# Kernel tuning notes

Hardware: AMD Instinct MI355X
Metric: run time of the kernel (lower is better)

The kernel has to match this reference:

```python
import jax, jax.numpy as jnp
import numpy as np

N = 100000
E = 1600000
F_IN = 512
HID = 8
HEADS = 8
NUM_CLASSES = 40
NEG_SLOPE = 0.2


def setup_inputs() -> dict:
    key = jax.random.key(0)
    ks = jax.random.split(key, 12)
    x = jax.random.normal(ks[0], (N, F_IN), dtype=jnp.float32)
    edge_index = jax.random.randint(ks[1], (2, E), 0, N, dtype=jnp.int64)
    s1 = 1.0 / np.sqrt(F_IN)
    s2 = 1.0 / np.sqrt(HID * HEADS)
    W1 = jax.random.normal(ks[2], (F_IN, HEADS * HID), dtype=jnp.float32) * s1
    a_src1 = jax.random.normal(ks[3], (HEADS, HID), dtype=jnp.float32) * s1
    a_dst1 = jax.random.normal(ks[4], (HEADS, HID), dtype=jnp.float32) * s1
    b1 = jnp.zeros((HEADS * HID,), dtype=jnp.float32)
    W2 = jax.random.normal(ks[5], (HEADS * HID, NUM_CLASSES), dtype=jnp.float32) * s2
    a_src2 = jax.random.normal(ks[6], (1, NUM_CLASSES), dtype=jnp.float32) * s2
    a_dst2 = jax.random.normal(ks[7], (1, NUM_CLASSES), dtype=jnp.float32) * s2
    b2 = jnp.zeros((NUM_CLASSES,), dtype=jnp.float32)
    return {"x": x, "edge_index": edge_index, "W1": W1, "a_src1": a_src1,
            "a_dst1": a_dst1, "b1": b1, "W2": W2, "a_src2": a_src2,
            "a_dst2": a_dst2, "b2": b2}


def _gat_conv(x, src, dst, W, a_src, a_dst, b, heads, out_ch):
    # linear projection, per-head: [N, heads, out_ch]
    h = (x @ W).reshape(N, heads, out_ch)
    # per-node attention logits [N, heads]
    al_s = jnp.einsum('nhf,hf->nh', h, a_src)
    al_d = jnp.einsum('nhf,hf->nh', h, a_dst)
    # per-edge raw scores [E', heads]
    e = jax.nn.leaky_relu(al_s[src] + al_d[dst], NEG_SLOPE)
    # segment softmax over edges sharing a destination node
    m = jax.lax.stop_gradient(jax.ops.segment_max(e, dst, num_segments=N))
    m = jnp.where(jnp.isfinite(m), m, 0.0)
    e = jnp.exp(e - m[dst])
    denom = jax.ops.segment_sum(e, dst, num_segments=N)
    alpha = e / denom[dst]  # [E', heads]
    # scatter-weighted aggregation of gathered source features
    out = jax.ops.segment_sum(alpha[:, :, None] * h[src], dst, num_segments=N)
    return out.reshape(N, heads * out_ch) + b


def reference(x, edge_index, W1, a_src1, a_dst1, b1, W2, a_src2, a_dst2, b2):
    # PyG GATConv default: add self-loops
    loops = jnp.arange(N, dtype=edge_index.dtype)
    src = jnp.concatenate([edge_index[0], loops])
    dst = jnp.concatenate([edge_index[1], loops])
    h = _gat_conv(x, src, dst, W1, a_src1, a_dst1, b1, HEADS, HID)
    h = jax.nn.elu(h)
    # dropout(p=0.6) is identity in eval mode
    out = _gat_conv(h, src, dst, W2, a_src2, a_dst2, b2, 1, NUM_CLASSES)
    return jax.nn.log_softmax(out, axis=1)
```

## Files before the change

kernel.cpp:

```cpp
#include <hip/hip_runtime.h>
#include <hip/hip_bf16.h>
#include <cstdint>
#include <cstddef>

#define N_NODES 100000
#define N_EDGES 1600000
#define E_TOT   (N_EDGES + N_NODES)
#define F_IN    512
#define HEADS   8
#define HID     8
#define F_H     64
#define NC      40
#define NEG     0.2f

#define BSH    8
#define NB     391
#define CHUNK  8192
#define NBLK_E ((E_TOT + CHUNK - 1) / CHUNK)
#define CAP    7168

typedef __attribute__((ext_vector_type(8))) __bf16 bf16x8;
typedef __attribute__((ext_vector_type(4))) float f32x4;
typedef __attribute__((ext_vector_type(8))) unsigned short u16x8;

__device__ __forceinline__ float bf2f(unsigned short u) {
  unsigned int w = ((unsigned int)u) << 16;
  return __builtin_bit_cast(float, w);
}
__device__ __forceinline__ unsigned short f2bf(float f) {
  __hip_bfloat16 b = __float2bfloat16(f);
  return __builtin_bit_cast(unsigned short, b);
}
__device__ __forceinline__ float lrexp(float v) {
  v = (v > 0.f) ? v : NEG * v;
  return __expf(v);
}

__global__ void k_detect(const int* __restrict__ ei, int* __restrict__ flag) {
  if (threadIdx.x == 0 && blockIdx.x == 0) {
    int nz = 0;
    for (int i = 0; i < 256; ++i) nz |= ei[2 * i + 1];
    *flag = (nz == 0) ? 1 : 0;
  }
}

__device__ __forceinline__ int load_dst(const int* __restrict__ ei, bool f, int i) {
  if (i < N_EDGES) return f ? ei[2 * (N_EDGES + i)] : ei[N_EDGES + i];
  return i - N_EDGES;
}
__device__ __forceinline__ int load_src(const int* __restrict__ ei, bool f, int i) {
  if (i < N_EDGES) return f ? ei[2 * i] : ei[i];
  return i - N_EDGES;
}

__global__ __launch_bounds__(256) void k_bhist(const int* __restrict__ ei,
                                               const int* __restrict__ flag,
                                               int* __restrict__ bcnt) {
  __shared__ int h[NB];
  const int t = threadIdx.x;
  for (int i = t; i < NB; i += 256) h[i] = 0;
  __syncthreads();
  const bool f = (*flag) != 0;
  const int base = blockIdx.x * CHUNK;
#pragma unroll
  for (int j = 0; j < CHUNK / 256; ++j) {
    int i = base + t + j * 256;
    if (i < E_TOT) atomicAdd(&h[load_dst(ei, f, i) >> BSH], 1);
  }
  __syncthreads();
  for (int i = t; i < NB; i += 256)
    if (h[i]) atomicAdd(&bcnt[i], h[i]);
}

__global__ __launch_bounds__(512) void k_bscan(const int* __restrict__ bcnt,
                                               int* __restrict__ bstart,
                                               int* __restrict__ bcur,
                                               int* __restrict__ rowstart) {
  __shared__ int sh[512];
  const int t = threadIdx.x;
  int v = (t < NB) ? bcnt[t] : 0;
  sh[t] = v;
  __syncthreads();
  for (int d = 1; d < 512; d <<= 1) {
    int u = (t >= d) ? sh[t - d] : 0;
    __syncthreads();
    sh[t] += u;
    __syncthreads();
  }
  if (t < NB) {
    int e = sh[t] - v;
    bstart[t] = e;
    bcur[t] = e;
  }
  if (t == 0) { bstart[NB] = E_TOT; rowstart[N_NODES] = E_TOT; }
}

__global__ __launch_bounds__(256) void k_bfill(const int* __restrict__ ei,
                                               const int* __restrict__ flag,
                                               int* __restrict__ bcur,
                                               unsigned int* __restrict__ inter) {
  __shared__ unsigned int ent[CHUNK];
  __shared__ int h[NB], ofs[NB], cur[NB], gpos[NB];
  const int t = threadIdx.x;
  const int base = blockIdx.x * CHUNK;
  const bool f = (*flag) != 0;
  for (int i = t; i < NB; i += 256) h[i] = 0;
  __syncthreads();
#pragma unroll
  for (int j = 0; j < CHUNK / 256; ++j) {
    int i = base + t + j * 256;
    if (i < E_TOT) atomicAdd(&h[load_dst(ei, f, i) >> BSH], 1);
  }
  __syncthreads();
  if (t < 64) {
    int loc[7];
    int s = 0;
#pragma unroll
    for (int k = 0; k < 7; ++k) {
      int idx = t * 7 + k;
      int hv = (idx < NB) ? h[idx] : 0;
      loc[k] = s;
      s += hv;
    }
    int incl = s;
    for (int dd = 1; dd < 64; dd <<= 1) {
      int u = __shfl_up(incl, dd);
      if (t >= dd) incl += u;
    }
    int excl = incl - s;
#pragma unroll
    for (int k = 0; k < 7; ++k) {
      int idx = t * 7 + k;
      if (idx < NB) ofs[idx] = excl + loc[k];
    }
  }
  __syncthreads();
  for (int i = t; i < NB; i += 256) {
    cur[i] = ofs[i];
    gpos[i] = h[i] ? atomicAdd(&bcur[i], h[i]) : 0;
  }
  __syncthreads();
#pragma unroll
  for (int j = 0; j < CHUNK / 256; ++j) {
    int i = base + t + j * 256;
    if (i < E_TOT) {
      int s = load_src(ei, f, i);
      int d = load_dst(ei, f, i);
      int p = atomicAdd(&cur[d >> BSH], 1);
      ent[p] = ((unsigned int)(d & 255) << 24) | (unsigned int)s;
    }
  }
  __syncthreads();
  const int wv = t >> 6, ln = t & 63;
  for (int b = wv; b < NB; b += 4) {
    int c = h[b];
    if (!c) continue;
    int g = gpos[b], o = ofs[b];
    for (int i = ln; i < c; i += 64) inter[g + i] = ent[o + i];
  }
}

__global__ __launch_bounds__(256) void k_cfill(const unsigned int* __restrict__ inter,
                                               const int* __restrict__ bstart,
                                               int* __restrict__ rowstart,
                                               int* __restrict__ csrc) {
  __shared__ unsigned int out_l[CAP];
  __shared__ int cnt[256], sc[256], cur2[256];
  const int t = threadIdx.x;
  const int b = blockIdx.x;
  const int segStart = bstart[b];
  const int L = bstart[b + 1] - segStart;
  cnt[t] = 0;
  __syncthreads();
  for (int i = t; i < L; i += 256) atomicAdd(&cnt[inter[segStart + i] >> 24], 1);
  __syncthreads();
  sc[t] = cnt[t];
  __syncthreads();
  for (int d = 1; d < 256; d <<= 1) {
    int v = (t >= d) ? sc[t - d] : 0;
    __syncthreads();
    sc[t] += v;
    __syncthreads();
  }
  const int excl = sc[t] - cnt[t];
  cur2[t] = excl;
  const int node = (b << BSH) + t;
  if (node < N_NODES) rowstart[node] = segStart + excl;
  __syncthreads();
  if (L <= CAP) {
    for (int i = t; i < L; i += 256) {
      unsigned int e = inter[segStart + i];
      int p = atomicAdd(&cur2[e >> 24], 1);
      out_l[p] = e & 0xFFFFFFu;
    }
    __syncthreads();
    for (int i = t; i < L; i += 256) csrc[segStart + i] = (int)out_l[i];
  } else {
    for (int i = t; i < L; i += 256) {
      unsigned int e = inter[segStart + i];
      int p = atomicAdd(&cur2[e >> 24], 1);
      csrc[segStart + p] = (int)(e & 0xFFFFFFu);
    }
  }
}

__global__ __launch_bounds__(256) void k_packW(const float* __restrict__ W1,
                                               uint4* __restrict__ w1f) {
  int tid = blockIdx.x * 256 + threadIdx.x;
  if (tid >= 4096) return;
  int lane = tid & 63;
  int t = (tid >> 6) & 3;
  int s = tid >> 8;
  int k0 = s * 32 + ((lane >> 4) << 3);
  int col = t * 16 + (lane & 15);
  u16x8 v;
#pragma unroll
  for (int i = 0; i < 8; ++i) v[i] = f2bf(W1[(size_t)(k0 + i) * F_H + col]);
  w1f[tid] = __builtin_bit_cast(uint4, v);
}

__global__ __launch_bounds__(256) void k_gemm1m(
    const float* __restrict__ x, const uint4* __restrict__ w1f,
    const float* __restrict__ a_src, const float* __restrict__ a_dst,
    unsigned short* __restrict__ h1b, float* __restrict__ als,
    float* __restrict__ ald) {
  const int t = threadIdx.x;
  const int lane = t & 63;
  const int wv = t >> 6;
  const int rb = blockIdx.x * 64 + wv * 16;
  int arow = rb + (lane & 15);
  if (arow >= N_NODES) arow = N_NODES - 1;
  const float* aptr = x + (size_t)arow * F_IN + ((lane >> 4) << 3);

  f32x4 acc[4];
#pragma unroll
  for (int i = 0; i < 4; ++i) acc[i] = (f32x4){0.f, 0.f, 0.f, 0.f};

#pragma unroll 4
  for (int s = 0; s < 16; ++s) {
    float4 a0 = *reinterpret_cast<const float4*>(aptr + s * 32);
    float4 a1 = *reinterpret_cast<const float4*>(aptr + s * 32 + 4);
    uint4 b0 = w1f[(s * 4 + 0) * 64 + lane];
    uint4 b1 = w1f[(s * 4 + 1) * 64 + lane];
    uint4 b2 = w1f[(s * 4 + 2) * 64 + lane];
    uint4 b3 = w1f[(s * 4 + 3) * 64 + lane];
    bf16x8 af;
    af[0] = (__bf16)a0.x; af[1] = (__bf16)a0.y;
    af[2] = (__bf16)a0.z; af[3] = (__bf16)a0.w;
    af[4] = (__bf16)a1.x; af[5] = (__bf16)a1.y;
    af[6] = (__bf16)a1.z; af[7] = (__bf16)a1.w;
    acc[0] = __builtin_amdgcn_mfma_f32_16x16x32_bf16(af, __builtin_bit_cast(bf16x8, b0), acc[0], 0, 0, 0);
    acc[1] = __builtin_amdgcn_mfma_f32_16x16x32_bf16(af, __builtin_bit_cast(bf16x8, b1), acc[1], 0, 0, 0);
    acc[2] = __builtin_amdgcn_mfma_f32_16x16x32_bf16(af, __builtin_bit_cast(bf16x8, b2), acc[2], 0, 0, 0);
    acc[3] = __builtin_amdgcn_mfma_f32_16x16x32_bf16(af, __builtin_bit_cast(bf16x8, b3), acc[3], 0, 0, 0);
  }

  const int r0 = rb + ((lane >> 4) << 2);
  const int c = lane & 15;
#pragma unroll
  for (int tt = 0; tt < 4; ++tt) {
#pragma unroll
    for (int i = 0; i < 4; ++i) {
      int r = r0 + i;
      if (r < N_NODES) h1b[(size_t)r * F_H + tt * 16 + c] = f2bf(acc[tt][i]);
    }
  }

  float asw[4], adw[4];
#pragma unroll
  for (int tt = 0; tt < 4; ++tt) {
    asw[tt] = a_src[tt * 16 + c];
    adw[tt] = a_dst[tt * 16 + c];
  }
  float sp[4][4], dp[4][4];
#pragma unroll
  for (int tt = 0; tt < 4; ++tt)
#pragma unroll
    for (int i = 0; i < 4; ++i) {
      sp[tt][i] = acc[tt][i] * asw[tt];
      dp[tt][i] = acc[tt][i] * adw[tt];
    }
#pragma unroll
  for (int dd = 1; dd < 8; dd <<= 1)
#pragma unroll
    for (int tt = 0; tt < 4; ++tt)
#pragma unroll
      for (int i = 0; i < 4; ++i) {
        sp[tt][i] += __shfl_xor(sp[tt][i], dd);
        dp[tt][i] += __shfl_xor(dp[tt][i], dd);
      }
  if ((c & 7) == 0) {
    const int hb = c >> 3;
#pragma unroll
    for (int i = 0; i < 4; ++i) {
      int r = r0 + i;
      if (r < N_NODES) {
#pragma unroll
        for (int tt = 0; tt < 4; ++tt) {
          als[(size_t)r * HEADS + tt * 2 + hb] = sp[tt][i];
          ald[(size_t)r * HEADS + tt * 2 + hb] = dp[tt][i];
        }
      }
    }
  }
}

__global__ __launch_bounds__(256) void k_agg1n(
    const int* __restrict__ rowstart, const int* __restrict__ csrc,
    const unsigned short* __restrict__ h1b, const float* __restrict__ als,
    const float* __restrict__ ald, const float* __restrict__ b1,
    unsigned short* __restrict__ hactb) {
  const int w = (int)((blockIdx.x * 256 + threadIdx.x) >> 6);
  const int lane = threadIdx.x & 63;
  const int grp = lane >> 3;
  const int l = lane & 7;
  const int n = w * 8 + grp;
  const bool live = (n < N_NODES);
  const int e0 = live ? rowstart[n] : 0;
  const int e1 = live ? rowstart[n + 1] : 0;
  const float aldv = live ? ald[(size_t)n * HEADS + l] : 0.f;

  float den = 0.f;
  float acc[8];
#pragma unroll
  for (int k = 0; k < 8; ++k) acc[k] = 0.f;

  int e = e0;
  for (; e + 4 <= e1; e += 4) {
    int4 sv = *reinterpret_cast<const int4*>(&csrc[e]);
    float a0 = als[(size_t)sv.x * HEADS + l];
    float a1 = als[(size_t)sv.y * HEADS + l];
    float a2 = als[(size_t)sv.z * HEADS + l];
    float a3 = als[(size_t)sv.w * HEADS + l];
    uint4 u0 = *reinterpret_cast<const uint4*>(&h1b[(size_t)sv.x * F_H + l * 8]);
    uint4 u1 = *reinterpret_cast<const uint4*>(&h1b[(size_t)sv.y * F_H + l * 8]);
    uint4 u2 = *reinterpret_cast<const uint4*>(&h1b[(size_t)sv.z * F_H + l * 8]);
    uint4 u3 = *reinterpret_cast<const uint4*>(&h1b[(size_t)sv.w * F_H + l * 8]);
    float p0 = lrexp(a0 + aldv), p1 = lrexp(a1 + aldv);
    float p2 = lrexp(a2 + aldv), p3 = lrexp(a3 + aldv);
    den += (p0 + p1) + (p2 + p3);
    const unsigned int* q0 = &u0.x;
    const unsigned int* q1 = &u1.x;
    const unsigned int* q2 = &u2.x;
    const unsigned int* q3 = &u3.x;
#pragma unroll
    for (int k = 0; k < 4; ++k) {
      acc[2 * k]     += p0 * bf2f((unsigned short)q0[k]) + p1 * bf2f((unsigned short)q1[k])
                      + p2 * bf2f((unsigned short)q2[k]) + p3 * bf2f((unsigned short)q3[k]);
      acc[2 * k + 1] += p0 * bf2f((unsigned short)(q0[k] >> 16)) + p1 * bf2f((unsigned short)(q1[k] >> 16))
                      + p2 * bf2f((unsigned short)(q2[k] >> 16)) + p3 * bf2f((unsigned short)(q3[k] >> 16));
    }
  }
  for (; e < e1; ++e) {
    int s = csrc[e];
    float a = als[(size_t)s * HEADS + l];
    uint4 u = *reinterpret_cast<const uint4*>(&h1b[(size_t)s * F_H + l * 8]);
    float p = lrexp(a + aldv);
    den += p;
    const unsigned int* q = &u.x;
#pragma unroll
    for (int k = 0; k < 4; ++k) {
      acc[2 * k]     += p * bf2f((unsigned short)q[k]);
      acc[2 * k + 1] += p * bf2f((unsigned short)(q[k] >> 16));
    }
  }

  if (live) {
    float inv = 1.f / den;
    uint4 outw;
    unsigned int* ow = &outw.x;
#pragma unroll
    for (int k = 0; k < 4; ++k) {
      float ox = acc[2 * k] * inv + b1[l * 8 + 2 * k];
      float oy = acc[2 * k + 1] * inv + b1[l * 8 + 2 * k + 1];
      ox = (ox > 0.f) ? ox : expm1f(ox);
      oy = (oy > 0.f) ? oy : expm1f(oy);
      ow[k] = ((unsigned int)f2bf(oy) << 16) | (unsigned int)f2bf(ox);
    }
    *reinterpret_cast<uint4*>(&hactb[(size_t)n * F_H + l * 8]) = outw;
  }
}

__global__ __launch_bounds__(256) void k_l2proj(
    const unsigned short* __restrict__ hactb, const float* __restrict__ W2,
    const float* __restrict__ a_src2, const float* __restrict__ a_dst2,
    unsigned short* __restrict__ h2b, float* __restrict__ als2,
    float* __restrict__ ald2) {
  __shared__ float hs[64 * 68];
  __shared__ float w2s[F_H * NC];
  const int t = threadIdx.x;
  const int nb = blockIdx.x * 64;
  {
    int r0 = t >> 3, c8 = t & 7;
#pragma unroll
    for (int i = 0; i < 2; ++i) {
      int r = r0 + i * 32;
      int gr = nb + r;
      u16x8 v = (u16x8)(0);
      if (gr < N_NODES)
        v = *reinterpret_cast<const u16x8*>(&hactb[(size_t)gr * F_H + c8 * 8]);
#pragma unroll
      for (int k = 0; k < 8; ++k) hs[r * 68 + c8 * 8 + k] = bf2f(v[k]);
    }
  }
  for (int i = t; i < F_H * NC; i += 256) w2s[i] = W2[i];
  __syncthreads();

  const int node = t >> 2, cg = t & 3;
  float acc[10];
#pragma unroll
  for (int c = 0; c < 10; ++c) acc[c] = 0.f;
  for (int k = 0; k < F_H; ++k) {
    float xv = hs[node * 68 + k];
#pragma unroll
    for (int c = 0; c < 10; ++c) acc[c] += xv * w2s[k * NC + cg * 10 + c];
  }
  const int gn = nb + node;
  float ps = 0.f, pd = 0.f;
#pragma unroll
  for (int c = 0; c < 10; ++c) {
    ps += acc[c] * a_src2[cg * 10 + c];
    pd += acc[c] * a_dst2[cg * 10 + c];
  }
  ps += __shfl_xor(ps, 1); ps += __shfl_xor(ps, 2);
  pd += __shfl_xor(pd, 1); pd += __shfl_xor(pd, 2);
  if (gn < N_NODES) {
#pragma unroll
    for (int c = 0; c < 10; ++c) h2b[(size_t)gn * NC + cg * 10 + c] = f2bf(acc[c]);
    if (cg == 0) { als2[gn] = ps; ald2[gn] = pd; }
  }
}

__global__ __launch_bounds__(256) void k_agg2n(
    const int* __restrict__ rowstart, const int* __restrict__ csrc,
    const unsigned short* __restrict__ h2b, const float* __restrict__ als2,
    const float* __restrict__ ald2, const float* __restrict__ b2,
    float* __restrict__ out) {
  const int w = (int)((blockIdx.x * 256 + threadIdx.x) >> 6);
  const int lane = threadIdx.x & 63;
  const int grp = lane >> 3;
  const int l = lane & 7;
  const int n = w * 8 + grp;
  const bool live = (n < N_NODES);
  const int e0 = live ? rowstart[n] : 0;
  const int e1 = live ? rowstart[n + 1] : 0;
  const float aldv = live ? ald2[n] : 0.f;
  const bool act = (l < 5);
  const int fo = act ? l * 8 : 0;

  float den = 0.f;
  float acc[8];
#pragma unroll
  for (int k = 0; k < 8; ++k) acc[k] = 0.f;

  int e = e0;
  for (; e + 4 <= e1; e += 4) {
    int4 sv = *reinterpret_cast<const int4*>(&csrc[e]);
    float a0 = als2[sv.x], a1 = als2[sv.y], a2 = als2[sv.z], a3 = als2[sv.w];
    uint4 u0 = *reinterpret_cast<const uint4*>(&h2b[(size_t)sv.x * NC + fo]);
    uint4 u1 = *reinterpret_cast<const uint4*>(&h2b[(size_t)sv.y * NC + fo]);
    uint4 u2 = *reinterpret_cast<const uint4*>(&h2b[(size_t)sv.z * NC + fo]);
    uint4 u3 = *reinterpret_cast<const uint4*>(&h2b[(size_t)sv.w * NC + fo]);
    float p0 = lrexp(a0 + aldv), p1 = lrexp(a1 + aldv);
    float p2 = lrexp(a2 + aldv), p3 = lrexp(a3 + aldv);
    den += (p0 + p1) + (p2 + p3);
    const unsigned int* q0 = &u0.x;
    const unsigned int* q1 = &u1.x;
    const unsigned int* q2 = &u2.x;
    const unsigned int* q3 = &u3.x;
#pragma unroll
    for (int k = 0; k < 4; ++k) {
      acc[2 * k]     += p0 * bf2f((unsigned short)q0[k]) + p1 * bf2f((unsigned short)q1[k])
                      + p2 * bf2f((unsigned short)q2[k]) + p3 * bf2f((unsigned short)q3[k]);
      acc[2 * k + 1] += p0 * bf2f((unsigned short)(q0[k] >> 16)) + p1 * bf2f((unsigned short)(q1[k] >> 16))
                      + p2 * bf2f((unsigned short)(q2[k] >> 16)) + p3 * bf2f((unsigned short)(q3[k] >> 16));
    }
  }
  for (; e < e1; ++e) {
    int s = csrc[e];
    float a = als2[s];
    uint4 u = *reinterpret_cast<const uint4*>(&h2b[(size_t)s * NC + fo]);
    float p = lrexp(a + aldv);
    den += p;
    const unsigned int* q = &u.x;
#pragma unroll
    for (int k = 0; k < 4; ++k) {
      acc[2 * k]     += p * bf2f((unsigned short)q[k]);
      acc[2 * k + 1] += p * bf2f((unsigned short)(q[k] >> 16));
    }
  }

  float o[8];
  float inv = 1.f / den;
  float mx = -1e30f;
#pragma unroll
  for (int k = 0; k < 8; ++k) {
    o[k] = act ? (acc[k] * inv + b2[fo + k]) : -1e30f;
    mx = fmaxf(mx, o[k]);
  }
  mx = fmaxf(mx, __shfl_xor(mx, 1));
  mx = fmaxf(mx, __shfl_xor(mx, 2));
  mx = fmaxf(mx, __shfl_xor(mx, 4));
  float se = 0.f;
#pragma unroll
  for (int k = 0; k < 8; ++k) se += act ? __expf(o[k] - mx) : 0.f;
  se += __shfl_xor(se, 1);
  se += __shfl_xor(se, 2);
  se += __shfl_xor(se, 4);
  if (live && act) {
    float ls = __logf(se);
    float4 r0, r1;
    r0.x = o[0] - mx - ls; r0.y = o[1] - mx - ls;
    r0.z = o[2] - mx - ls; r0.w = o[3] - mx - ls;
    r1.x = o[4] - mx - ls; r1.y = o[5] - mx - ls;
    r1.z = o[6] - mx - ls; r1.w = o[7] - mx - ls;
    *reinterpret_cast<float4*>(&out[(size_t)n * NC + l * 8]) = r0;
    *reinterpret_cast<float4*>(&out[(size_t)n * NC + l * 8 + 4]) = r1;
  }
}

extern "C" void kernel_launch(void* const* d_in, const int* in_sizes, int n_in,
                              void* d_out, int out_size, void* d_ws, size_t ws_size,
                              hipStream_t stream) {
  const float* x      = (const float*)d_in[0];
  const int*   ei     = (const int*)d_in[1];
  const float* W1     = (const float*)d_in[2];
  const float* a_src1 = (const float*)d_in[3];
  const float* a_dst1 = (const float*)d_in[4];
  const float* b1     = (const float*)d_in[5];
  const float* W2     = (const float*)d_in[6];
  const float* a_src2 = (const float*)d_in[7];
  const float* a_dst2 = (const float*)d_in[8];
  const float* b2     = (const float*)d_in[9];
  float* out = (float*)d_out;

  char* ws = (char*)d_ws;
  size_t o = 0;
  auto carve = [&](size_t bytes) -> char* {
    char* p = ws + o;
    o = (o + bytes + 255) & ~(size_t)255;
    return p;
  };
  int*   flag     = (int*)carve(256);
  int*   bcnt     = (int*)carve((size_t)NB * 4);
  int*   bstart   = (int*)carve((size_t)(NB + 1) * 4);
  int*   bcur     = (int*)carve((size_t)NB * 4);
  int*   rowstart = (int*)carve((size_t)(N_NODES + 1) * 4);
  unsigned int* inter = (unsigned int*)carve((size_t)E_TOT * 4);
  int*   csrc     = (int*)carve((size_t)(E_TOT + 8) * 4);
  uint4* w1f      = (uint4*)carve((size_t)4096 * 16);
  unsigned short* h1b   = (unsigned short*)carve((size_t)N_NODES * F_H * 2);
  float* als1     = (float*)carve((size_t)N_NODES * HEADS * 4);
  float* ald1     = (float*)carve((size_t)N_NODES * HEADS * 4);
  unsigned short* hactb = (unsigned short*)carve((size_t)N_NODES * F_H * 2);
  unsigned short* h2b   = (unsigned short*)carve((size_t)(N_NODES * NC + 8) * 2);
  float* als2     = (float*)carve((size_t)N_NODES * 4);
  float* ald2     = (float*)carve((size_t)N_NODES * 4);
  (void)ws_size; (void)n_in; (void)in_sizes; (void)out_size;

  hipMemsetAsync(bcnt, 0, (size_t)NB * 4, stream);
  k_detect<<<1, 64, 0, stream>>>(ei, flag);
  k_bhist<<<NBLK_E, 256, 0, stream>>>(ei, flag, bcnt);
  k_bscan<<<1, 512, 0, stream>>>(bcnt, bstart, bcur, rowstart);
  k_bfill<<<NBLK_E, 256, 0, stream>>>(ei, flag, bcur, inter);
  k_cfill<<<NB, 256, 0, stream>>>(inter, bstart, rowstart, csrc);

  k_packW<<<16, 256, 0, stream>>>(W1, w1f);
  k_gemm1m<<<(N_NODES + 63) / 64, 256, 0, stream>>>(x, w1f, a_src1, a_dst1, h1b, als1, ald1);

  const int aggGrid = (N_NODES + 31) / 32;
  k_agg1n<<<aggGrid, 256, 0, stream>>>(rowstart, csrc, h1b, als1, ald1, b1, hactb);
  k_l2proj<<<(N_NODES + 63) / 64, 256, 0, stream>>>(hactb, W2, a_src2, a_dst2, h2b, als2, ald2);
  k_agg2n<<<aggGrid, 256, 0, stream>>>(rowstart, csrc, h2b, als2, ald2, b2, out);
}
```

Measured before the change: 282.3 us.

## Fuse edge bucket fill with layer-1 GEMM and histogram with weight packing

```diff
diff --git a/kernel.cpp b/kernel.cpp
--- a/kernel.cpp
+++ b/kernel.cpp
@@ -15,9 +15,14 @@
 
 #define BSH    8
 #define NB     391
-#define CHUNK  8192
-#define NBLK_E ((E_TOT + CHUNK - 1) / CHUNK)
+#define CHUNKH 8192
+#define NBH    ((E_TOT + CHUNKH - 1) / CHUNKH)
+#define CHUNKF 4096
+#define NBF    ((E_TOT + CHUNKF - 1) / CHUNKF)
 #define CAP    7168
+#define GEMM_G ((N_NODES + 63) / 64)
+#define FG_T   (GEMM_G + NBF)
+#define FG_R1  (NBF * 4)
 
 typedef __attribute__((ext_vector_type(8))) __bf16 bf16x8;
 typedef __attribute__((ext_vector_type(4))) float f32x4;
@@ -36,12 +41,10 @@
   return __expf(v);
 }
 
-__global__ void k_detect(const int* __restrict__ ei, int* __restrict__ flag) {
-  if (threadIdx.x == 0 && blockIdx.x == 0) {
-    int nz = 0;
-    for (int i = 0; i < 256; ++i) nz |= ei[2 * i + 1];
-    *flag = (nz == 0) ? 1 : 0;
-  }
+__device__ __forceinline__ bool detect_i64(const int* __restrict__ ei) {
+  int lane = threadIdx.x & 63;
+  int v = ei[2 * lane + 1];
+  return __ballot(v != 0) == 0ull;
 }
 
 __device__ __forceinline__ int load_dst(const int* __restrict__ ei, bool f, int i) {
@@ -53,17 +56,31 @@
   return i - N_EDGES;
 }
 
-__global__ __launch_bounds__(256) void k_bhist(const int* __restrict__ ei,
-                                               const int* __restrict__ flag,
-                                               int* __restrict__ bcnt) {
+__global__ __launch_bounds__(256) void k_hist_pack(
+    const int* __restrict__ ei, const float* __restrict__ W1,
+    uint4* __restrict__ w1f, int* __restrict__ bcnt) {
   __shared__ int h[NB];
   const int t = threadIdx.x;
+  if (blockIdx.x < 16) {
+    int tid = blockIdx.x * 256 + t;
+    int lane = tid & 63;
+    int tt = (tid >> 6) & 3;
+    int s = tid >> 8;
+    int k0 = s * 32 + ((lane >> 4) << 3);
+    int col = tt * 16 + (lane & 15);
+    u16x8 v;
+#pragma unroll
+    for (int i = 0; i < 8; ++i) v[i] = f2bf(W1[(size_t)(k0 + i) * F_H + col]);
+    w1f[tid] = __builtin_bit_cast(uint4, v);
+    return;
+  }
+  const int blk = blockIdx.x - 16;
+  const bool f = detect_i64(ei);
   for (int i = t; i < NB; i += 256) h[i] = 0;
   __syncthreads();
-  const bool f = (*flag) != 0;
-  const int base = blockIdx.x * CHUNK;
-#pragma unroll
-  for (int j = 0; j < CHUNK / 256; ++j) {
+  const int base = blk * CHUNKH;
+#pragma unroll
+  for (int j = 0; j < CHUNKH / 256; ++j) {
     int i = base + t + j * 256;
     if (i < E_TOT) atomicAdd(&h[load_dst(ei, f, i) >> BSH], 1);
   }
@@ -95,139 +112,89 @@
   if (t == 0) { bstart[NB] = E_TOT; rowstart[N_NODES] = E_TOT; }
 }
 
-__global__ __launch_bounds__(256) void k_bfill(const int* __restrict__ ei,
-                                               const int* __restrict__ flag,
-                                               int* __restrict__ bcur,
-                                               unsigned int* __restrict__ inter) {
-  __shared__ unsigned int ent[CHUNK];
-  __shared__ int h[NB], ofs[NB], cur[NB], gpos[NB];
-  const int t = threadIdx.x;
-  const int base = blockIdx.x * CHUNK;
-  const bool f = (*flag) != 0;
-  for (int i = t; i < NB; i += 256) h[i] = 0;
-  __syncthreads();
-#pragma unroll
-  for (int j = 0; j < CHUNK / 256; ++j) {
-    int i = base + t + j * 256;
-    if (i < E_TOT) atomicAdd(&h[load_dst(ei, f, i) >> BSH], 1);
-  }
-  __syncthreads();
-  if (t < 64) {
-    int loc[7];
-    int s = 0;
-#pragma unroll
-    for (int k = 0; k < 7; ++k) {
-      int idx = t * 7 + k;
-      int hv = (idx < NB) ? h[idx] : 0;
-      loc[k] = s;
-      s += hv;
-    }
-    int incl = s;
-    for (int dd = 1; dd < 64; dd <<= 1) {
-      int u = __shfl_up(incl, dd);
-      if (t >= dd) incl += u;
-    }
-    int excl = incl - s;
-#pragma unroll
-    for (int k = 0; k < 7; ++k) {
-      int idx = t * 7 + k;
-      if (idx < NB) ofs[idx] = excl + loc[k];
-    }
-  }
-  __syncthreads();
-  for (int i = t; i < NB; i += 256) {
-    cur[i] = ofs[i];
-    gpos[i] = h[i] ? atomicAdd(&bcur[i], h[i]) : 0;
-  }
-  __syncthreads();
-#pragma unroll
-  for (int j = 0; j < CHUNK / 256; ++j) {
-    int i = base + t + j * 256;
-    if (i < E_TOT) {
-      int s = load_src(ei, f, i);
-      int d = load_dst(ei, f, i);
-      int p = atomicAdd(&cur[d >> BSH], 1);
-      ent[p] = ((unsigned int)(d & 255) << 24) | (unsigned int)s;
-    }
-  }
-  __syncthreads();
-  const int wv = t >> 6, ln = t & 63;
-  for (int b = wv; b < NB; b += 4) {
-    int c = h[b];
-    if (!c) continue;
-    int g = gpos[b], o = ofs[b];
-    for (int i = ln; i < c; i += 64) inter[g + i] = ent[o + i];
-  }
-}
-
-__global__ __launch_bounds__(256) void k_cfill(const unsigned int* __restrict__ inter,
-                                               const int* __restrict__ bstart,
-                                               int* __restrict__ rowstart,
-                                               int* __restrict__ csrc) {
-  __shared__ unsigned int out_l[CAP];
-  __shared__ int cnt[256], sc[256], cur2[256];
-  const int t = threadIdx.x;
-  const int b = blockIdx.x;
-  const int segStart = bstart[b];
-  const int L = bstart[b + 1] - segStart;
-  cnt[t] = 0;
-  __syncthreads();
-  for (int i = t; i < L; i += 256) atomicAdd(&cnt[inter[segStart + i] >> 24], 1);
-  __syncthreads();
-  sc[t] = cnt[t];
-  __syncthreads();
-  for (int d = 1; d < 256; d <<= 1) {
-    int v = (t >= d) ? sc[t - d] : 0;
-    __syncthreads();
-    sc[t] += v;
-    __syncthreads();
-  }
-  const int excl = sc[t] - cnt[t];
-  cur2[t] = excl;
-  const int node = (b << BSH) + t;
-  if (node < N_NODES) rowstart[node] = segStart + excl;
-  __syncthreads();
-  if (L <= CAP) {
-    for (int i = t; i < L; i += 256) {
-      unsigned int e = inter[segStart + i];
-      int p = atomicAdd(&cur2[e >> 24], 1);
-      out_l[p] = e & 0xFFFFFFu;
-    }
-    __syncthreads();
-    for (int i = t; i < L; i += 256) csrc[segStart + i] = (int)out_l[i];
-  } else {
-    for (int i = t; i < L; i += 256) {
-      unsigned int e = inter[segStart + i];
-      int p = atomicAdd(&cur2[e >> 24], 1);
-      csrc[segStart + p] = (int)(e & 0xFFFFFFu);
-    }
-  }
-}
-
-__global__ __launch_bounds__(256) void k_packW(const float* __restrict__ W1,
-                                               uint4* __restrict__ w1f) {
-  int tid = blockIdx.x * 256 + threadIdx.x;
-  if (tid >= 4096) return;
-  int lane = tid & 63;
-  int t = (tid >> 6) & 3;
-  int s = tid >> 8;
-  int k0 = s * 32 + ((lane >> 4) << 3);
-  int col = t * 16 + (lane & 15);
-  u16x8 v;
-#pragma unroll
-  for (int i = 0; i < 8; ++i) v[i] = f2bf(W1[(size_t)(k0 + i) * F_H + col]);
-  w1f[tid] = __builtin_bit_cast(uint4, v);
-}
-
-__global__ __launch_bounds__(256) void k_gemm1m(
+__global__ __launch_bounds__(256) void k_fill_gemm(
+    const int* __restrict__ ei, int* __restrict__ bcur,
+    unsigned int* __restrict__ inter,
     const float* __restrict__ x, const uint4* __restrict__ w1f,
     const float* __restrict__ a_src, const float* __restrict__ a_dst,
     unsigned short* __restrict__ h1b, float* __restrict__ als,
     float* __restrict__ ald) {
+  __shared__ unsigned int ent[CHUNKF];
+  __shared__ int h[NB], ofs[NB], cur[NB], gpos[NB];
+  const int b = (int)blockIdx.x;
   const int t = threadIdx.x;
+  bool isFill;
+  int idx;
+  if (b < FG_R1) {
+    if ((b & 3) == 3) { isFill = true;  idx = b >> 2; }
+    else              { isFill = false; idx = b - (b >> 2); }
+  } else {
+    isFill = false; idx = b - NBF;
+  }
+
+  if (isFill) {
+    const bool f = detect_i64(ei);
+    const int base = idx * CHUNKF;
+    for (int i = t; i < NB; i += 256) h[i] = 0;
+    __syncthreads();
+#pragma unroll
+    for (int j = 0; j < CHUNKF / 256; ++j) {
+      int i = base + t + j * 256;
+      if (i < E_TOT) atomicAdd(&h[load_dst(ei, f, i) >> BSH], 1);
+    }
+    __syncthreads();
+    if (t < 64) {
+      int loc[7];
+      int s = 0;
+#pragma unroll
+      for (int k = 0; k < 7; ++k) {
+        int ix = t * 7 + k;
+        int hv = (ix < NB) ? h[ix] : 0;
+        loc[k] = s;
+        s += hv;
+      }
+      int incl = s;
+      for (int dd = 1; dd < 64; dd <<= 1) {
+        int u = __shfl_up(incl, dd);
+        if (t >= dd) incl += u;
+      }
+      int excl = incl - s;
+#pragma unroll
+      for (int k = 0; k < 7; ++k) {
+        int ix = t * 7 + k;
+        if (ix < NB) ofs[ix] = excl + loc[k];
+      }
+    }
+    __syncthreads();
+    for (int i = t; i < NB; i += 256) {
+      cur[i] = ofs[i];
+      gpos[i] = h[i] ? atomicAdd(&bcur[i], h[i]) : 0;
+    }
+    __syncthreads();
+#pragma unroll
+    for (int j = 0; j < CHUNKF / 256; ++j) {
+      int i = base + t + j * 256;
+      if (i < E_TOT) {
+        int s = load_src(ei, f, i);
+        int d = load_dst(ei, f, i);
+        int p = atomicAdd(&cur[d >> BSH], 1);
+        ent[p] = ((unsigned int)(d & 255) << 24) | (unsigned int)s;
+      }
+    }
+    __syncthreads();
+    const int wv = t >> 6, ln = t & 63;
+    for (int bb = wv; bb < NB; bb += 4) {
+      int c = h[bb];
+      if (!c) continue;
+      int g = gpos[bb], o = ofs[bb];
+      for (int i = ln; i < c; i += 64) inter[g + i] = ent[o + i];
+    }
+    return;
+  }
+
   const int lane = t & 63;
   const int wv = t >> 6;
-  const int rb = blockIdx.x * 64 + wv * 16;
+  const int rb = idx * 64 + wv * 16;
   int arow = rb + (lane & 15);
   if (arow >= N_NODES) arow = N_NODES - 1;
   const float* aptr = x + (size_t)arow * F_IN + ((lane >> 4) << 3);
@@ -301,6 +268,50 @@
           ald[(size_t)r * HEADS + tt * 2 + hb] = dp[tt][i];
         }
       }
+    }
+  }
+}
+
+__global__ __launch_bounds__(256) void k_cfill(const unsigned int* __restrict__ inter,
+                                               const int* __restrict__ bstart,
+                                               int* __restrict__ rowstart,
+                                               int* __restrict__ csrc) {
+  __shared__ unsigned int out_l[CAP];
+  __shared__ int cnt[256], sc[256], cur2[256];
+  const int t = threadIdx.x;
+  const int b = blockIdx.x;
+  const int segStart = bstart[b];
+  const int L = bstart[b + 1] - segStart;
+  cnt[t] = 0;
+  __syncthreads();
+  for (int i = t; i < L; i += 256) atomicAdd(&cnt[inter[segStart + i] >> 24], 1);
+  __syncthreads();
+  sc[t] = cnt[t];
+  __syncthreads();
+  for (int d = 1; d < 256; d <<= 1) {
+    int v = (t >= d) ? sc[t - d] : 0;
+    __syncthreads();
+    sc[t] += v;
+    __syncthreads();
+  }
+  const int excl = sc[t] - cnt[t];
+  cur2[t] = excl;
+  const int node = (b << BSH) + t;
+  if (node < N_NODES) rowstart[node] = segStart + excl;
+  __syncthreads();
+  if (L <= CAP) {
+    for (int i = t; i < L; i += 256) {
+      unsigned int e = inter[segStart + i];
+      int p = atomicAdd(&cur2[e >> 24], 1);
+      out_l[p] = e & 0xFFFFFFu;
+    }
+    __syncthreads();
+    for (int i = t; i < L; i += 256) csrc[segStart + i] = (int)out_l[i];
+  } else {
+    for (int i = t; i < L; i += 256) {
+      unsigned int e = inter[segStart + i];
+      int p = atomicAdd(&cur2[e >> 24], 1);
+      csrc[segStart + p] = (int)(e & 0xFFFFFFu);
     }
   }
 }
@@ -541,7 +552,6 @@
     o = (o + bytes + 255) & ~(size_t)255;
     return p;
   };
-  int*   flag     = (int*)carve(256);
   int*   bcnt     = (int*)carve((size_t)NB * 4);
   int*   bstart   = (int*)carve((size_t)(NB + 1) * 4);
   int*   bcur     = (int*)carve((size_t)NB * 4);
@@ -559,14 +569,11 @@
   (void)ws_size; (void)n_in; (void)in_sizes; (void)out_size;
 
   hipMemsetAsync(bcnt, 0, (size_t)NB * 4, stream);
-  k_detect<<<1, 64, 0, stream>>>(ei, flag);
-  k_bhist<<<NBLK_E, 256, 0, stream>>>(ei, flag, bcnt);
+  k_hist_pack<<<16 + NBH, 256, 0, stream>>>(ei, W1, w1f, bcnt);
   k_bscan<<<1, 512, 0, stream>>>(bcnt, bstart, bcur, rowstart);
-  k_bfill<<<NBLK_E, 256, 0, stream>>>(ei, flag, bcur, inter);
+  k_fill_gemm<<<FG_T, 256, 0, stream>>>(ei, bcur, inter, x, w1f, a_src1, a_dst1,
+                                        h1b, als1, ald1);
   k_cfill<<<NB, 256, 0, stream>>>(inter, bstart, rowstart, csrc);
-
-  k_packW<<<16, 256, 0, stream>>>(W1, w1f);
-  k_gemm1m<<<(N_NODES + 63) / 64, 256, 0, stream>>>(x, w1f, a_src1, a_dst1, h1b, als1, ald1);
 
   const int aggGrid = (N_NODES + 31) / 32;
   k_agg1n<<<aggGrid, 256, 0, stream>>>(rowstart, csrc, h1b, als1, ald1, b1, hactb);
```

Result: faster. 246.4 us (-12.7%).
